# Optimization experiments

Hardware: AMD Instinct MI355X
Metric: run time of the kernel (lower is better)

Reference implementation:

```python
import jax, jax.numpy as jnp
import numpy as np

EPS = 1e-5

def setup_inputs() -> dict:
    key = jax.random.key(0)
    k1, k2, k3, k4, k5 = jax.random.split(key, 5)
    x = jax.random.normal(k1, (2048, 64, 768), dtype=jnp.float32)
    ln_w = jnp.ones((768,), dtype=jnp.float32)
    ln_b = jnp.zeros((768,), dtype=jnp.float32)
    # nn.Linear default init: U(-1/sqrt(in), 1/sqrt(in))
    bound = 1.0 / np.sqrt(768.0)
    W = jax.random.uniform(k2, (64, 768), dtype=jnp.float32, minval=-bound, maxval=bound)
    b = jax.random.uniform(k3, (64,), dtype=jnp.float32, minval=-bound, maxval=bound)
    return {"x": x, "ln_w": ln_w, "ln_b": ln_b, "W": W, "b": b}

def reference(x, ln_w, ln_b, W, b):
    B = x.shape[0]
    # LayerNorm over last dim (768)
    mu = jnp.mean(x, axis=-1, keepdims=True)
    var = jnp.mean(jnp.square(x - mu), axis=-1, keepdims=True)
    xn = (x - mu) * jax.lax.rsqrt(var + EPS) * ln_w + ln_b
    # Linear 768 -> 64, then SiLU
    y = jnp.einsum('bch,oh->bco', xn, W) + b
    y = y * jax.nn.sigmoid(y)
    # unpatchify: [B,64,64] -> [B,8,8,4,4,4] -> permute(0,3,1,4,2,5) -> [B,4,32,32]
    y = y.reshape(B, 8, 8, 4, 4, 4)
    y = jnp.transpose(y, (0, 3, 1, 4, 2, 5))
    return y.reshape(B, 4, 32, 32)
```

## Files before the change

kernel.cpp:

```cpp
#include <hip/hip_runtime.h>
#include <hip/hip_bf16.h>
#include <cstdint>

typedef __attribute__((ext_vector_type(8))) short s16x8;
typedef __attribute__((ext_vector_type(4))) float f32x4;

union CV2 { __hip_bfloat162 h; uint32_t u; };

__global__ void prep_kernel(const float* __restrict__ W,
                            const float* __restrict__ lnw,
                            const float* __restrict__ lnb,
                            const float* __restrict__ bias,
                            __hip_bfloat16* __restrict__ Wb,
                            float* __restrict__ Ssum,
                            float* __restrict__ bp) {
    const int o = blockIdx.x;
    const int tid = threadIdx.x;
    float s = 0.f, bb = 0.f;
    for (int k = tid; k < 768; k += 256) {
        float wraw = W[o * 768 + k];
        float wv = lnw[k] * wraw;
        s += wv;
        bb += lnb[k] * wraw;
        int kk = k >> 5, rem = k & 31;
        int q = rem >> 3, j = rem & 7;
        int t = o >> 4, n = o & 15;
        int l = q * 16 + n;
        Wb[(kk * 4 + t) * 512 + l * 8 + j] = __float2bfloat16(wv);
    }
    __shared__ float rs[4], rb[4];
    for (int off = 32; off > 0; off >>= 1) {
        s  += __shfl_down(s, off);
        bb += __shfl_down(bb, off);
    }
    int wid = tid >> 6;
    if ((tid & 63) == 0) { rs[wid] = s; rb[wid] = bb; }
    __syncthreads();
    if (tid == 0) {
        Ssum[o] = rs[0] + rs[1] + rs[2] + rs[3];
        bp[o]   = bias[o] + rb[0] + rb[1] + rb[2] + rb[3];
    }
}

__global__ __launch_bounds__(256, 3) void fused_kernel(
        const float* __restrict__ x,
        const uint4* __restrict__ Wb4,
        const float* __restrict__ Ssum,
        const float* __restrict__ bp,
        float* __restrict__ out) {
    const int b   = blockIdx.x;
    const int tid = threadIdx.x;
    const int w   = tid >> 6;
    const int l   = tid & 63;
    const int q   = l >> 4;
    const int n   = l & 15;

    __shared__ __align__(16) char lds[2 * 17408];

    const float* xb = x + (size_t)b * 49152;
    const int srow = tid >> 5;
    const int u    = tid & 31;

    float4 st[8];
    #pragma unroll
    for (int j = 0; j < 8; j++)
        st[j] = *(const float4*)(xb + (j * 8 + srow) * 768 + u * 4);
    #pragma unroll
    for (int j = 0; j < 8; j++) {
        CV2 lo, hi;
        lo.h = __float22bfloat162_rn(make_float2(st[j].x, st[j].y));
        hi.h = __float22bfloat162_rn(make_float2(st[j].z, st[j].w));
        *(uint2*)(lds + (j * 8 + srow) * 272 + u * 8) = make_uint2(lo.u, hi.u);
    }
    __syncthreads();

    f32x4 acc0 = {0.f, 0.f, 0.f, 0.f};
    f32x4 acc1 = acc0, acc2 = acc0, acc3 = acc0;
    float sum = 0.f, ssq = 0.f;
    const uint4* wbl = Wb4 + l;

    #pragma unroll
    for (int c = 0; c < 6; c++) {
        if (c < 5) {
            #pragma unroll
            for (int j = 0; j < 8; j++)
                st[j] = *(const float4*)(xb + (j * 8 + srow) * 768
                                         + (c + 1) * 128 + u * 4);
        }

        const char* bufp = lds + (c & 1) * 17408 + (w * 16 + n) * 272 + q * 16;
        uint4 fr[4];
        #pragma unroll
        for (int s = 0; s < 4; s++) fr[s] = *(const uint4*)(bufp + s * 64);

        const uint4* wpc = wbl + c * 1024;
        uint4 wb0 = wpc[0], wb1 = wpc[64], wb2 = wpc[128], wb3 = wpc[192];

        #pragma unroll
        for (int s = 0; s < 4; s++) {
            uint4 nb0, nb1, nb2, nb3;
            if (s < 3) {
                const uint4* wp = wpc + (s + 1) * 256;
                nb0 = wp[0]; nb1 = wp[64]; nb2 = wp[128]; nb3 = wp[192];
            }
            union { uint4 u4; unsigned short us[8]; } fu; fu.u4 = fr[s];
            #pragma unroll
            for (int j = 0; j < 8; j++) {
                float xv = __uint_as_float(((unsigned)fu.us[j]) << 16);
                sum += xv;
                ssq = fmaf(xv, xv, ssq);
            }
            s16x8 af = __builtin_bit_cast(s16x8, fr[s]);
            acc0 = __builtin_amdgcn_mfma_f32_16x16x32_bf16(
                       af, __builtin_bit_cast(s16x8, wb0), acc0, 0, 0, 0);
            acc1 = __builtin_amdgcn_mfma_f32_16x16x32_bf16(
                       af, __builtin_bit_cast(s16x8, wb1), acc1, 0, 0, 0);
            acc2 = __builtin_amdgcn_mfma_f32_16x16x32_bf16(
                       af, __builtin_bit_cast(s16x8, wb2), acc2, 0, 0, 0);
            acc3 = __builtin_amdgcn_mfma_f32_16x16x32_bf16(
                       af, __builtin_bit_cast(s16x8, wb3), acc3, 0, 0, 0);
            if (s < 3) { wb0 = nb0; wb1 = nb1; wb2 = nb2; wb3 = nb3; }
        }

        if (c < 5) {
            char* obuf = lds + ((c + 1) & 1) * 17408;
            #pragma unroll
            for (int j = 0; j < 8; j++) {
                CV2 lo, hi;
                lo.h = __float22bfloat162_rn(make_float2(st[j].x, st[j].y));
                hi.h = __float22bfloat162_rn(make_float2(st[j].z, st[j].w));
                *(uint2*)(obuf + (j * 8 + srow) * 272 + u * 8) =
                    make_uint2(lo.u, hi.u);
            }
        }
        __syncthreads();
    }

    sum += __shfl_xor(sum, 16); sum += __shfl_xor(sum, 32);
    ssq += __shfl_xor(ssq, 16); ssq += __shfl_xor(ssq, 32);
    const float mu   = sum * (1.0f / 768.0f);
    const float rstd = rsqrtf(ssq * (1.0f / 768.0f) - mu * mu + 1e-5f);

    float St[4], Bt[4];
    #pragma unroll
    for (int t = 0; t < 4; t++) {
        St[t] = Ssum[t * 16 + n];
        Bt[t] = bp[t * 16 + n];
    }

    float* sout = (float*)lds;
    const int o2 = (n >> 2) & 3;
    const int o3 = n & 3;
    f32x4 va[4] = {acc0, acc1, acc2, acc3};
    #pragma unroll
    for (int r = 0; r < 4; r++) {
        float mu_r   = __shfl(mu,   q * 4 + r);
        float rstd_r = __shfl(rstd, q * 4 + r);
        int cc  = w * 16 + q * 4 + r;
        int c1i = cc >> 3, c2i = cc & 7;
        int base = (c1i * 4 + o2) * 32 + c2i * 4 + o3;
        #pragma unroll
        for (int t = 0; t < 4; t++) {
            float y = rstd_r * (va[t][r] - mu_r * St[t]) + Bt[t];
            y = y / (1.0f + __expf(-y));
            sout[t * 1024 + base] = y;
        }
    }
    __syncthreads();

    float* outp = out + (size_t)b * 4096;
    #pragma unroll
    for (int j = 0; j < 4; j++) {
        *(float4*)(outp + j * 1024 + tid * 4) =
            *(const float4*)(&sout[j * 1024 + tid * 4]);
    }
}

extern "C" void kernel_launch(void* const* d_in, const int* in_sizes, int n_in,
                              void* d_out, int out_size, void* d_ws, size_t ws_size,
                              hipStream_t stream) {
    const float* x    = (const float*)d_in[0];
    const float* lnw  = (const float*)d_in[1];
    const float* lnb  = (const float*)d_in[2];
    const float* W    = (const float*)d_in[3];
    const float* bias = (const float*)d_in[4];
    float* out = (float*)d_out;

    const int B = in_sizes[0] / (64 * 768);

    __hip_bfloat16* Wb = (__hip_bfloat16*)d_ws;
    float* Ssum = (float*)((char*)d_ws + 98304);
    float* bp   = (float*)((char*)d_ws + 98304 + 256);

    prep_kernel<<<64, 256, 0, stream>>>(W, lnw, lnb, bias, Wb, Ssum, bp);
    fused_kernel<<<B, 256, 0, stream>>>(x, (const uint4*)d_ws, Ssum, bp, out);
}
```

Before: 559.7 us.

## Stage weight tiles through LDS and prefetch x and weights two chunks ahead

Per-wave global loads of bf16 weight fragments are replaced by a cooperative block load of each 16KB weight chunk into a double-buffered LDS region, read back by every wave. The global prefetch of x (and now weights) is issued after the LDS store of the previous chunk, so loads run two chunks ahead across the barrier. The aim is to cut redundant L2 weight traffic and hide global latency. In exchange LDS use grows to about 67KB per block and launch bounds drop from 3 to 2 blocks per CU, which lowers occupancy.

```diff
diff --git a/kernel.cpp b/kernel.cpp
--- a/kernel.cpp
+++ b/kernel.cpp
@@ -42,7 +42,7 @@
     }
 }
 
-__global__ __launch_bounds__(256, 3) void fused_kernel(
+__global__ __launch_bounds__(256, 2) void fused_kernel(
         const float* __restrict__ x,
         const uint4* __restrict__ Wb4,
         const float* __restrict__ Ssum,
@@ -55,16 +55,21 @@
     const int q   = l >> 4;
     const int n   = l & 15;
 
-    __shared__ __align__(16) char lds[2 * 17408];
+    __shared__ __align__(16) char lds[2 * 17408 + 2 * 16384];
 
     const float* xb = x + (size_t)b * 49152;
     const int srow = tid >> 5;
     const int u    = tid & 31;
 
     float4 st[8];
+    uint4  wst[4];
+
     #pragma unroll
     for (int j = 0; j < 8; j++)
         st[j] = *(const float4*)(xb + (j * 8 + srow) * 768 + u * 4);
+    #pragma unroll
+    for (int j = 0; j < 4; j++)
+        wst[j] = Wb4[tid + j * 256];
     #pragma unroll
     for (int j = 0; j < 8; j++) {
         CV2 lo, hi;
@@ -72,37 +77,33 @@
         hi.h = __float22bfloat162_rn(make_float2(st[j].z, st[j].w));
         *(uint2*)(lds + (j * 8 + srow) * 272 + u * 8) = make_uint2(lo.u, hi.u);
     }
+    #pragma unroll
+    for (int j = 0; j < 4; j++)
+        *(uint4*)(lds + 34816 + (tid + j * 256) * 16) = wst[j];
+
+    #pragma unroll
+    for (int j = 0; j < 8; j++)
+        st[j] = *(const float4*)(xb + (j * 8 + srow) * 768 + 128 + u * 4);
+    #pragma unroll
+    for (int j = 0; j < 4; j++)
+        wst[j] = Wb4[1024 + tid + j * 256];
     __syncthreads();
 
     f32x4 acc0 = {0.f, 0.f, 0.f, 0.f};
     f32x4 acc1 = acc0, acc2 = acc0, acc3 = acc0;
     float sum = 0.f, ssq = 0.f;
-    const uint4* wbl = Wb4 + l;
 
     #pragma unroll
     for (int c = 0; c < 6; c++) {
-        if (c < 5) {
-            #pragma unroll
-            for (int j = 0; j < 8; j++)
-                st[j] = *(const float4*)(xb + (j * 8 + srow) * 768
-                                         + (c + 1) * 128 + u * 4);
-        }
-
-        const char* bufp = lds + (c & 1) * 17408 + (w * 16 + n) * 272 + q * 16;
+        const char* xbp = lds + (c & 1) * 17408 + (w * 16 + n) * 272 + q * 16;
         uint4 fr[4];
         #pragma unroll
-        for (int s = 0; s < 4; s++) fr[s] = *(const uint4*)(bufp + s * 64);
-
-        const uint4* wpc = wbl + c * 1024;
-        uint4 wb0 = wpc[0], wb1 = wpc[64], wb2 = wpc[128], wb3 = wpc[192];
+        for (int s = 0; s < 4; s++) fr[s] = *(const uint4*)(xbp + s * 64);
+
+        const char* wbp = lds + 34816 + (c & 1) * 16384 + l * 16;
 
         #pragma unroll
         for (int s = 0; s < 4; s++) {
-            uint4 nb0, nb1, nb2, nb3;
-            if (s < 3) {
-                const uint4* wp = wpc + (s + 1) * 256;
-                nb0 = wp[0]; nb1 = wp[64]; nb2 = wp[128]; nb3 = wp[192];
-            }
             union { uint4 u4; unsigned short us[8]; } fu; fu.u4 = fr[s];
             #pragma unroll
             for (int j = 0; j < 8; j++) {
@@ -110,6 +111,10 @@
                 sum += xv;
                 ssq = fmaf(xv, xv, ssq);
             }
+            uint4 wb0 = *(const uint4*)(wbp + (s * 4 + 0) * 1024);
+            uint4 wb1 = *(const uint4*)(wbp + (s * 4 + 1) * 1024);
+            uint4 wb2 = *(const uint4*)(wbp + (s * 4 + 2) * 1024);
+            uint4 wb3 = *(const uint4*)(wbp + (s * 4 + 3) * 1024);
             s16x8 af = __builtin_bit_cast(s16x8, fr[s]);
             acc0 = __builtin_amdgcn_mfma_f32_16x16x32_bf16(
                        af, __builtin_bit_cast(s16x8, wb0), acc0, 0, 0, 0);
@@ -119,21 +124,33 @@
                        af, __builtin_bit_cast(s16x8, wb2), acc2, 0, 0, 0);
             acc3 = __builtin_amdgcn_mfma_f32_16x16x32_bf16(
                        af, __builtin_bit_cast(s16x8, wb3), acc3, 0, 0, 0);
-            if (s < 3) { wb0 = nb0; wb1 = nb1; wb2 = nb2; wb3 = nb3; }
         }
 
         if (c < 5) {
-            char* obuf = lds + ((c + 1) & 1) * 17408;
+            char* xo = lds + ((c + 1) & 1) * 17408;
+            char* wo = lds + 34816 + ((c + 1) & 1) * 16384;
             #pragma unroll
             for (int j = 0; j < 8; j++) {
                 CV2 lo, hi;
                 lo.h = __float22bfloat162_rn(make_float2(st[j].x, st[j].y));
                 hi.h = __float22bfloat162_rn(make_float2(st[j].z, st[j].w));
-                *(uint2*)(obuf + (j * 8 + srow) * 272 + u * 8) =
+                *(uint2*)(xo + (j * 8 + srow) * 272 + u * 8) =
                     make_uint2(lo.u, hi.u);
             }
+            #pragma unroll
+            for (int j = 0; j < 4; j++)
+                *(uint4*)(wo + (tid + j * 256) * 16) = wst[j];
+            if (c < 4) {
+                #pragma unroll
+                for (int j = 0; j < 8; j++)
+                    st[j] = *(const float4*)(xb + (j * 8 + srow) * 768
+                                             + (c + 2) * 128 + u * 4);
+                #pragma unroll
+                for (int j = 0; j < 4; j++)
+                    wst[j] = Wb4[(c + 2) * 1024 + tid + j * 256];
+            }
+            __syncthreads();
         }
-        __syncthreads();
     }
 
     sum += __shfl_xor(sum, 16); sum += __shfl_xor(sum, 32);
```

Result: faster. 547.6 us (-2.2%).
